# Kernel optimization log

Hardware: AMD Instinct MI355X
Metric: run time of the kernel (lower is better)

## Reference

```python
import jax, jax.numpy as jnp
import numpy as np

B = 65536
NQ = 8
NL = 3
FEAT = 64 * 3 * 3 + NQ  # 584


def _conv(x, w, b):
    # x: (B,C,H,W), w: (O,I,3,3), padding=1 -> SAME
    y = jax.lax.conv_general_dilated(
        x, w, window_strides=(1, 1), padding='SAME',
        dimension_numbers=('NCHW', 'OIHW', 'NCHW'))
    return y + b[None, :, None, None]


def _maxpool2(x):
    return jax.lax.reduce_window(
        x, -jnp.inf, jax.lax.max, (1, 1, 2, 2), (1, 1, 2, 2), 'VALID')


def _quantum_sim(x, qp):
    # x: (B,NQ); qp: (NL,NQ,3). Within a layer, qubit q depends only on its own
    # previous state (tanh term), so vectorize over qubits and scan over layers.
    x_next = jnp.roll(x, -1, axis=1)  # x[:, (q+1) % NQ]

    def step(q_state, rot):  # rot: (NQ,3)
        new = jnp.sin(rot[:, 0] * x) * jnp.cos(rot[:, 1] * x_next) \
              + jnp.tanh(rot[:, 2] * q_state)
        return new, None

    q0 = jnp.zeros_like(x)
    qf, _ = jax.lax.scan(step, q0, qp)
    return qf


def setup_inputs() -> dict:
    key = jax.random.key(0)
    ks = jax.random.split(key, 16)

    def w(k, shape, fan_in):
        lim = 1.0 / np.sqrt(fan_in)
        return jax.random.uniform(k, shape, jnp.float32, -lim, lim)

    return {
        'board_state': jax.random.normal(ks[0], (B, 3, 6, 6), jnp.float32),
        'target_positions': jax.random.randint(ks[1], (4, 2), 0, 6).astype(jnp.int64),
        'conv1_w': w(ks[2], (16, 3, 3, 3), 3 * 9), 'conv1_b': w(ks[3], (16,), 3 * 9),
        'conv2_w': w(ks[4], (32, 16, 3, 3), 16 * 9), 'conv2_b': w(ks[5], (32,), 16 * 9),
        'conv3_w': w(ks[6], (64, 32, 3, 3), 32 * 9), 'conv3_b': w(ks[7], (64,), 32 * 9),
        'quantum_params': jax.random.normal(ks[8], (NL, NQ, 3), jnp.float32),
        'pt_w1': w(ks[9], (FEAT, 128), FEAT), 'pt_b1': w(ks[9], (128,), FEAT),
        'pt_w2': w(ks[10], (128, 64), 128), 'pt_b2': w(ks[10], (64,), 128),
        'pt_w3': w(ks[11], (64, 2), 64), 'pt_b3': w(ks[11], (2,), 64),
        'cf_w1': w(ks[12], (FEAT, 64), FEAT), 'cf_b1': w(ks[12], (64,), FEAT),
        'cf_w2': w(ks[13], (64, 1), 64), 'cf_b2': w(ks[13], (1,), 64),
    }


def reference(board_state, target_positions,
              conv1_w, conv1_b, conv2_w, conv2_b, conv3_w, conv3_b,
              quantum_params,
              pt_w1, pt_b1, pt_w2, pt_b2, pt_w3, pt_b3,
              cf_w1, cf_b1, cf_w2, cf_b2):
    b = board_state.shape[0]
    h = jax.nn.relu(_conv(board_state, conv1_w, conv1_b))   # (B,16,6,6)
    h = jax.nn.relu(_conv(h, conv2_w, conv2_b))             # (B,32,6,6)
    h = _maxpool2(h)                                        # (B,32,3,3)
    h = jax.nn.relu(_conv(h, conv3_w, conv3_b))             # (B,64,3,3)
    conv_flat = h.reshape(b, -1)                            # (B,576)

    board_flat = board_state.reshape(b, -1)
    q_feat = _quantum_sim(board_flat[:, :NQ], quantum_params)  # (B,NQ)

    feats = jnp.concatenate([conv_flat, q_feat], axis=1)    # (B,584)

    # piece-type head (Dropout is identity in eval)
    t = jax.nn.relu(feats @ pt_w1 + pt_b1)
    t = jax.nn.relu(t @ pt_w2 + pt_b2)
    type_logits = t @ pt_w3 + pt_b3
    type_probs = jax.nn.softmax(type_logits, axis=1)        # (B,2)

    # confidence head
    c = jax.nn.relu(feats @ cf_w1 + cf_b1)
    confidence = jax.nn.sigmoid(c @ cf_w2 + cf_b2)          # (B,1)

    # target_positions never affect the math (pos_encoding unused in torch source);
    # the same probs/confidence are reported for every position.
    return jnp.concatenate([type_probs, confidence], axis=1)  # (B,3)
```

## Files before the change

kernel.cpp:

```cpp
#include <hip/hip_runtime.h>

typedef _Float16 h8 __attribute__((ext_vector_type(8)));
typedef _Float16 h4 __attribute__((ext_vector_type(4)));
typedef float f32x4 __attribute__((ext_vector_type(4)));

union HU { _Float16 h; unsigned short u; };
__device__ __forceinline__ unsigned short f2h(float f) { HU x; x.h = (_Float16)f; return x.u; }
__device__ __forceinline__ float h2f(unsigned short u) { HU x; x.u = u; return (float)x.h; }

#define MFMA16(a, b, c) __builtin_amdgcn_mfma_f32_16x16x32_f16((a), (b), (c), 0, 0, 0)

__global__ void k_prep(const float* __restrict__ w1, const float* __restrict__ w2,
                       const float* __restrict__ w3,
                       const float* __restrict__ ptw1, const float* __restrict__ cfw1,
                       const float* __restrict__ ptw2, const float* __restrict__ ptw3,
                       const float* __restrict__ cfw2,
                       unsigned short* __restrict__ w1f,
                       unsigned short* __restrict__ w2f,
                       unsigned short* __restrict__ w3f,
                       unsigned short* __restrict__ w1hd,
                       unsigned short* __restrict__ w2hd,
                       unsigned short* __restrict__ w3hd) {
    int gid = blockIdx.x * 256 + threadIdx.x;
    int gs = gridDim.x * 256;
    for (int e = gid; e < 1024; e += gs) {
        int f = e >> 9, lane = (e >> 3) & 63, j = e & 7;
        int k = ((lane >> 4) << 3) + j, oc = lane & 15;
        int r, within;
        if (f == 0) { r = k >> 4; within = k & 15; }
        else        { r = 2;      within = k; }
        int tx = within >> 2, ch = within & 3;
        float v = 0.f;
        if (tx < 3 && ch < 3) v = w1[oc * 27 + ch * 9 + r * 3 + tx];
        w1f[e] = f2h(v);
    }
    for (int e = gid; e < 9216; e += gs) {
        int j = e & 7, lane = (e >> 3) & 63, fo = e >> 9;
        int ot = fo & 1, t = fo >> 1;
        int k = ((lane >> 4) * 8) + j, oc = ot * 16 + (lane & 15);
        float v = (k < 16) ? w2[oc * 144 + k * 9 + t] : 0.f;
        w2f[e] = f2h(v);
    }
    for (int e = gid; e < 18432; e += gs) {
        int j = e & 7, lane = (e >> 3) & 63, fo = e >> 9;
        int oti = fo & 1, t = (fo >> 1) % 9, otp = (fo >> 1) / 9;
        int ic = ((lane >> 4) * 8) + j, oc = (otp * 2 + oti) * 16 + (lane & 15);
        w3f[e] = f2h(w3[oc * 288 + ic * 9 + t]);
    }
    for (int s = gid; s < 608 * 192; s += gs) {
        int k = s / 192, n = s - k * 192;
        float v = 0.f;
        if (k < 584) {
            int f = (k < 576) ? ((k & 63) * 9 + (k >> 6)) : k;
            v = (n < 128) ? ptw1[f * 128 + n] : cfw1[f * 64 + (n - 128)];
        }
        int kk = k >> 5, hi = (k & 31) >> 3, j = k & 7, nt = n >> 4;
        int e = (((kk * 12 + nt) << 6) | (hi << 4) | (n & 15)) << 3 | j;
        w1hd[e] = f2h(v);
    }
    for (int s = gid; s < 8192; s += gs) {
        int k = s >> 6, n = s & 63;
        float v = ptw2[k * 64 + n];
        int kk = k >> 5, hi = (k & 31) >> 3, j = k & 7, nt = n >> 4;
        int e = ((((kk << 2) | nt) << 6) | (hi << 4) | (n & 15)) << 3 | j;
        w2hd[e] = f2h(v);
    }
    for (int e = gid; e < 2048; e += gs) {
        int j = e & 7, lane = (e >> 3) & 63, kk = e >> 9;
        int k = kk * 32 + ((lane >> 4) * 8) + j, n = lane & 15;
        float v = 0.f;
        if (k < 64) { if (n < 2) v = ptw3[k * 2 + n]; }
        else        { if (n == 2) v = cfw2[k - 64]; }
        w3hd[e] = f2h(v);
    }
}

#define BDS4 260
#define BDH4 (16 * BDS4)
#define A1S 584
#define A2S 296
#define FTS 616
#define HSH 200
#define RA_OFF 19712
#define O_OFF 26112
#define LDSTOT 26368

__global__ __launch_bounds__(256, 3) void k_fused(
    const float* __restrict__ board,
    const float* __restrict__ b1, const float* __restrict__ b2,
    const float* __restrict__ b3, const float* __restrict__ qp,
    const unsigned short* __restrict__ w1f,
    const unsigned short* __restrict__ w2f,
    const unsigned short* __restrict__ w3f,
    const unsigned short* __restrict__ w1hd,
    const unsigned short* __restrict__ w2hd,
    const unsigned short* __restrict__ w3hd,
    const float* __restrict__ ptb1, const float* __restrict__ ptb2,
    const float* __restrict__ ptb3, const float* __restrict__ cfb1,
    const float* __restrict__ cfb2,
    float* __restrict__ out)
{
    __shared__ __align__(16) unsigned short LDSH[LDSTOT];
    const int tid = threadIdx.x, wid = tid >> 6, lane = tid & 63;
    const int g = wid >> 1, w2 = wid & 1;
    const int col = lane & 15, q = lane >> 4;
    const long long gg0 = (long long)blockIdx.x * 32;
    const f32x4 ZERO4 = {0.f, 0.f, 0.f, 0.f};

    unsigned short* A1 = LDSH + g * 9856;
    unsigned short* A2 = A1;
    unsigned short* Hb = LDSH + RA_OFF;
    float* O = (float*)(LDSH + O_OFF);

    for (int e = tid; e < BDH4 / 4; e += 256)
        ((unsigned long long*)(LDSH + RA_OFF))[e] = 0ULL;
    __syncthreads();

    float qv[2];
    h8 w1r0 = ((const h8*)w1f)[lane];
    h8 w1r1 = ((const h8*)w1f)[64 + lane];
    float b1v = b1[col];
    #pragma unroll
    for (int gi = 0; gi < 2; gi++) {
        for (int e = tid; e < 16 * 108; e += 256) {
            int ss = e / 108, r2 = e % 108, ch = r2 / 36, p = r2 % 36;
            float v = board[(gg0 + gi * 16) * 108 + e];
            LDSH[RA_OFF + ss * BDS4 + ((p / 6 + 1) * 8 + (p % 6) + 1) * 4 + ch] =
                f2h(v);
        }
        __syncthreads();
        if (tid < 128) {
            int ss = tid >> 3, qq = tid & 7;
            int base = RA_OFF + ss * BDS4;
            int p8a = ((qq / 6 + 1) * 8 + (qq % 6) + 1) * 4;
            int e2 = (qq + 1) & 7;
            int p8b = ((e2 / 6 + 1) * 8 + (e2 % 6) + 1) * 4;
            float xq = h2f(LDSH[base + p8a]);
            float xn = h2f(LDSH[base + p8b]);
            float st = 0.f;
            for (int l = 0; l < 3; l++) {
                float a0 = qp[l * 24 + qq * 3], a1 = qp[l * 24 + qq * 3 + 1],
                      a2 = qp[l * 24 + qq * 3 + 2];
                st = sinf(a0 * xq) * cosf(a1 * xn) + tanhf(a2 * st);
            }
            qv[gi] = st;
        }
        {
            unsigned short* A1g = LDSH + gi * 9856;
            const int bs = RA_OFF + col * BDS4;
            const int rsel = q >> 1, wo = (q & 1) * 8;
            for (int p = wid * 9; p < wid * 9 + 9; p++) {
                int y = p / 6, x = p % 6;
                int ab1 = bs + ((y + rsel) * 8 + x) * 4 + wo;
                int ab2 = bs + ((y + 2) * 8 + x) * 4 + wo;
                union { h8 v; h4 h[2]; } a1v, a2v;
                a1v.h[0] = *(const h4*)&LDSH[ab1];
                a1v.h[1] = *(const h4*)&LDSH[ab1 + 4];
                a2v.h[0] = *(const h4*)&LDSH[ab2];
                a2v.h[1] = *(const h4*)&LDSH[ab2 + 4];
                f32x4 c = MFMA16(a1v.v, w1r0, ZERO4);
                c = MFMA16(a2v.v, w1r1, c);
                #pragma unroll
                for (int r = 0; r < 4; r++)
                    A1g[(q * 4 + r) * A1S + p * 16 + col] =
                        f2h(fmaxf(c[r] + b1v, 0.f));
            }
        }
        __syncthreads();
    }

    f32x4 pooled2[9];
    #pragma unroll
    for (int pp = 0; pp < 9; pp++) pooled2[pp] = ZERO4;
    {
        h8 W2r[9];
        #pragma unroll
        for (int t = 0; t < 9; t++)
            W2r[t] = ((const h8*)w2f)[(t * 2 + w2) * 64 + lane];
        float b2v = b2[w2 * 16 + col];
        const int sA1 = col * A1S;
        const int kho = (q & 1) * 8;

        h8 R[3][6];
        #pragma unroll
        for (int x = 0; x < 6; x++) {
            R[0][x] = *(const h8*)&A1[sA1 + (0 * 6 + x) * 16 + kho];
            R[1][x] = *(const h8*)&A1[sA1 + (1 * 6 + x) * 16 + kho];
        }
        #pragma unroll
        for (int y = 0; y < 6; y++) {
            if (y >= 1 && y <= 4) {
                const int nr = y + 1, slot = nr % 3;
                #pragma unroll
                for (int x = 0; x < 6; x++)
                    R[slot][x] = *(const h8*)&A1[sA1 + (nr * 6 + x) * 16 + kho];
            }
            f32x4 acc[6];
            #pragma unroll
            for (int x = 0; x < 6; x++) acc[x] = ZERO4;
            #pragma unroll
            for (int dy = -1; dy <= 1; dy++) {
                const int ry = y + dy;
                if (ry < 0 || ry > 5) continue;
                const int slot = ry % 3;
                #pragma unroll
                for (int x = 0; x < 6; x++)
                    #pragma unroll
                    for (int dx = -1; dx <= 1; dx++) {
                        const int sx = x + dx;
                        if (sx < 0 || sx > 5) continue;
                        acc[x] = MFMA16(R[slot][sx],
                                        W2r[(dy + 1) * 3 + (dx + 1)], acc[x]);
                    }
            }
            const int pr = y >> 1;
            #pragma unroll
            for (int px = 0; px < 3; px++)
                #pragma unroll
                for (int xx = 0; xx < 2; xx++)
                    #pragma unroll
                    for (int r = 0; r < 4; r++)
                        pooled2[pr * 3 + px][r] =
                            fmaxf(pooled2[pr * 3 + px][r],
                                  acc[px * 2 + xx][r] + b2v);
        }
    }
    __syncthreads();
    #pragma unroll
    for (int pp = 0; pp < 9; pp++)
        #pragma unroll
        for (int r = 0; r < 4; r++)
            A2[(q * 4 + r) * A2S + pp * 32 + w2 * 16 + col] =
                f2h(pooled2[pp][r]);
    __syncthreads();

    f32x4 c3a[9], c3b[9];
    {
        const int otp = w2;
        const int sA2 = col * A2S;
        h8 W3r[18];
        #pragma unroll
        for (int f = 0; f < 18; f++)
            W3r[f] = ((const h8*)w3f)[(otp * 18 + f) * 64 + lane];
        #pragma unroll
        for (int p = 0; p < 9; p++) {
            const int y = p / 3, x = p % 3;
            f32x4 acc0 = ZERO4, acc1 = ZERO4;
            #pragma unroll
            for (int t = 0; t < 9; t++) {
                const int sy = y + t / 3 - 1, sx = x + t % 3 - 1;
                if (sy < 0 || sy >= 3 || sx < 0 || sx >= 3) continue;
                h8 a = *(const h8*)&A2[sA2 + (sy * 3 + sx) * 32 + q * 8];
                acc0 = MFMA16(a, W3r[t * 2 + 0], acc0);
                acc1 = MFMA16(a, W3r[t * 2 + 1], acc1);
            }
            c3a[p] = acc0; c3b[p] = acc1;
        }
    }
    __syncthreads();

    {
        const int otp = w2;
        float b3v0 = b3[(otp * 2 + 0) * 16 + col];
        float b3v1 = b3[(otp * 2 + 1) * 16 + col];
        int oc0 = (otp * 2 + 0) * 16 + col, oc1 = (otp * 2 + 1) * 16 + col;
        #pragma unroll
        for (int p = 0; p < 9; p++)
            #pragma unroll
            for (int r = 0; r < 4; r++) {
                int row = g * 16 + q * 4 + r;
                LDSH[row * FTS + p * 64 + oc0] = f2h(fmaxf(c3a[p][r] + b3v0, 0.f));
                LDSH[row * FTS + p * 64 + oc1] = f2h(fmaxf(c3b[p][r] + b3v1, 0.f));
            }
        if (tid < 128) {
            int ss = tid >> 3, qq = tid & 7;
            LDSH[ss * FTS + 576 + qq] = f2h(qv[0]);
            LDSH[(ss + 16) * FTS + 576 + qq] = f2h(qv[1]);
        }
        for (int e = tid; e < 1024; e += 256)
            LDSH[(e >> 5) * FTS + 584 + (e & 31)] = 0;
    }
    __syncthreads();

    {
        f32x4 acc[2][3];
        #pragma unroll
        for (int mt = 0; mt < 2; mt++)
            #pragma unroll
            for (int nt = 0; nt < 3; nt++) acc[mt][nt] = ZERO4;
        const h8* wp1 = (const h8*)w1hd;
        const int ntb = wid * 3;
        for (int kk = 0; kk < 19; kk++) {
            h8 a0 = *(const h8*)&LDSH[col * FTS + kk * 32 + q * 8];
            h8 a1 = *(const h8*)&LDSH[(16 + col) * FTS + kk * 32 + q * 8];
            h8 b[3];
            #pragma unroll
            for (int nt = 0; nt < 3; nt++)
                b[nt] = wp1[(kk * 12 + ntb + nt) * 64 + lane];
            #pragma unroll
            for (int nt = 0; nt < 3; nt++) {
                acc[0][nt] = MFMA16(a0, b[nt], acc[0][nt]);
                acc[1][nt] = MFMA16(a1, b[nt], acc[1][nt]);
            }
        }
        #pragma unroll
        for (int nt = 0; nt < 3; nt++) {
            int ntg = ntb + nt;
            float bv = (ntg < 8) ? ptb1[ntg * 16 + col] : cfb1[(ntg - 8) * 16 + col];
            #pragma unroll
            for (int mt = 0; mt < 2; mt++)
                #pragma unroll
                for (int r = 0; r < 4; r++)
                    Hb[(mt * 16 + q * 4 + r) * HSH + ntg * 16 + col] =
                        f2h(fmaxf(acc[mt][nt][r] + bv, 0.f));
        }
    }
    __syncthreads();

    {
        f32x4 acc2[2];
        acc2[0] = ZERO4; acc2[1] = ZERO4;
        const h8* wp2 = (const h8*)w2hd;
        const int nt2 = wid;
        #pragma unroll
        for (int kk = 0; kk < 4; kk++) {
            h8 a0 = *(const h8*)&Hb[col * HSH + kk * 32 + q * 8];
            h8 a1 = *(const h8*)&Hb[(16 + col) * HSH + kk * 32 + q * 8];
            h8 b = wp2[(kk * 4 + nt2) * 64 + lane];
            acc2[0] = MFMA16(a0, b, acc2[0]);
            acc2[1] = MFMA16(a1, b, acc2[1]);
        }
        __syncthreads();
        float bv2 = ptb2[nt2 * 16 + col];
        #pragma unroll
        for (int mt = 0; mt < 2; mt++)
            #pragma unroll
            for (int r = 0; r < 4; r++)
                Hb[(mt * 16 + q * 4 + r) * HSH + nt2 * 16 + col] =
                    f2h(fmaxf(acc2[mt][r] + bv2, 0.f));
    }
    __syncthreads();

    if (wid < 2) {
        const int mt = wid;
        f32x4 a3 = ZERO4;
        #pragma unroll
        for (int kk = 0; kk < 4; kk++) {
            int base = (kk < 2) ? kk * 32 : kk * 32 + 64;
            h8 a = *(const h8*)&Hb[(mt * 16 + col) * HSH + base + q * 8];
            h8 b = ((const h8*)w3hd)[kk * 64 + lane];
            a3 = MFMA16(a, b, a3);
        }
        if (col < 3) {
            float bv = (col < 2) ? ptb3[col] : cfb2[0];
            #pragma unroll
            for (int r = 0; r < 4; r++)
                O[(mt * 16 + q * 4 + r) * 4 + col] = a3[r] + bv;
        }
        if (lane < 16) {
            int s = mt * 16 + lane;
            float l0 = O[s * 4 + 0], l1 = O[s * 4 + 1], l2 = O[s * 4 + 2];
            float m = fmaxf(l0, l1);
            float e0 = expf(l0 - m), e1 = expf(l1 - m);
            float inv = 1.f / (e0 + e1);
            float* op = out + (gg0 + s) * 3;
            op[0] = e0 * inv;
            op[1] = e1 * inv;
            op[2] = 1.f / (1.f + expf(-l2));
        }
    }
}

extern "C" void kernel_launch(void* const* d_in, const int* in_sizes, int n_in,
                              void* d_out, int out_size, void* d_ws, size_t ws_size,
                              hipStream_t stream) {
    const float* board = (const float*)d_in[0];
    const float* c1w  = (const float*)d_in[2];
    const float* c1b  = (const float*)d_in[3];
    const float* c2w  = (const float*)d_in[4];
    const float* c2b  = (const float*)d_in[5];
    const float* c3w  = (const float*)d_in[6];
    const float* c3b  = (const float*)d_in[7];
    const float* qp   = (const float*)d_in[8];
    const float* ptw1 = (const float*)d_in[9];
    const float* ptb1 = (const float*)d_in[10];
    const float* ptw2 = (const float*)d_in[11];
    const float* ptb2 = (const float*)d_in[12];
    const float* ptw3 = (const float*)d_in[13];
    const float* ptb3 = (const float*)d_in[14];
    const float* cfw1 = (const float*)d_in[15];
    const float* cfb1 = (const float*)d_in[16];
    const float* cfw2 = (const float*)d_in[17];
    const float* cfb2 = (const float*)d_in[18];
    float* out = (float*)d_out;

    int Btot = in_sizes[0] / 108;

    unsigned short* w1f   = (unsigned short*)d_ws;
    unsigned short* w2f   = (unsigned short*)((char*)d_ws + 2048);
    unsigned short* w3f   = (unsigned short*)((char*)d_ws + 20480);
    unsigned short* w1hd  = (unsigned short*)((char*)d_ws + 57344);
    unsigned short* w2hd  = (unsigned short*)((char*)d_ws + 290816);
    unsigned short* w3hd  = (unsigned short*)((char*)d_ws + 307200);

    hipLaunchKernelGGL(k_prep, dim3(256), dim3(256), 0, stream,
                       c1w, c2w, c3w, ptw1, cfw1, ptw2, ptw3, cfw2,
                       w1f, w2f, w3f, w1hd, w2hd, w3hd);
    hipLaunchKernelGGL(k_fused, dim3(Btot / 32), dim3(256), 0, stream,
                       board, c1b, c2b, c3b, qp, w1f, w2f, w3f,
                       w1hd, w2hd, w3hd, ptb1, ptb2, ptb3, cfb1, cfb2, out);
}
```

Baseline: 175.6 us.

## Use 512-thread blocks and 32x32 MFMA for conv2 with fused pooling

Doubles the block to 8 waves and reassigns work across all stages. Conv2 now uses 32x32x16 MFMA with the 32 samples as the M dimension and K=16 input channels, so the zero-padded half of the K dimension is no longer computed. Each wave computes one pooled output position, and wave 0 also takes the ninth. Conv3 and the head GEMMs are split so each wave handles a single output or row tile. The aim is more parallelism per block and less wasted MFMA work. In exchange, conv2 no longer reuses rows through registers and the work is unevenly balanced across waves, with wave 0 doing double duty.

```diff
diff --git a/kernel.cpp b/kernel.cpp
--- a/kernel.cpp
+++ b/kernel.cpp
@@ -3,12 +3,14 @@
 typedef _Float16 h8 __attribute__((ext_vector_type(8)));
 typedef _Float16 h4 __attribute__((ext_vector_type(4)));
 typedef float f32x4 __attribute__((ext_vector_type(4)));
+typedef float f32x16 __attribute__((ext_vector_type(16)));
 
 union HU { _Float16 h; unsigned short u; };
 __device__ __forceinline__ unsigned short f2h(float f) { HU x; x.h = (_Float16)f; return x.u; }
 __device__ __forceinline__ float h2f(unsigned short u) { HU x; x.u = u; return (float)x.h; }
 
 #define MFMA16(a, b, c) __builtin_amdgcn_mfma_f32_16x16x32_f16((a), (b), (c), 0, 0, 0)
+#define MFMA32(a, b, c) __builtin_amdgcn_mfma_f32_32x32x16_f16((a), (b), (c), 0, 0, 0)
 
 __global__ void k_prep(const float* __restrict__ w1, const float* __restrict__ w2,
                        const float* __restrict__ w3,
@@ -34,12 +36,10 @@
         if (tx < 3 && ch < 3) v = w1[oc * 27 + ch * 9 + r * 3 + tx];
         w1f[e] = f2h(v);
     }
-    for (int e = gid; e < 9216; e += gs) {
-        int j = e & 7, lane = (e >> 3) & 63, fo = e >> 9;
-        int ot = fo & 1, t = fo >> 1;
-        int k = ((lane >> 4) * 8) + j, oc = ot * 16 + (lane & 15);
-        float v = (k < 16) ? w2[oc * 144 + k * 9 + t] : 0.f;
-        w2f[e] = f2h(v);
+    for (int e = gid; e < 4608; e += gs) {
+        int j = e & 7, lane = (e >> 3) & 63, t = e >> 9;
+        int oc = lane & 31, k = ((lane >> 5) << 3) + j;
+        w2f[e] = f2h(w2[oc * 144 + k * 9 + t]);
     }
     for (int e = gid; e < 18432; e += gs) {
         int j = e & 7, lane = (e >> 3) & 63, fo = e >> 9;
@@ -85,7 +85,40 @@
 #define O_OFF 26112
 #define LDSTOT 26368
 
-__global__ __launch_bounds__(256, 3) void k_fused(
+__device__ __forceinline__ f32x16 conv2_pool(const unsigned short* __restrict__ Ab,
+                                             const h8 (&W2r)[9], int kh, float b2v,
+                                             int pr, int pc) {
+    f32x16 pool;
+    #pragma unroll
+    for (int r = 0; r < 16; r++) pool[r] = 0.f;
+    #pragma unroll
+    for (int sy = 0; sy < 2; sy++)
+        #pragma unroll
+        for (int sx = 0; sx < 2; sx++) {
+            const int oy = pr * 2 + sy, ox = pc * 2 + sx;
+            f32x16 acc;
+            #pragma unroll
+            for (int r = 0; r < 16; r++) acc[r] = 0.f;
+            #pragma unroll
+            for (int dy = -1; dy <= 1; dy++) {
+                const int ry = oy + dy;
+                if (ry < 0 || ry > 5) continue;
+                #pragma unroll
+                for (int dx = -1; dx <= 1; dx++) {
+                    const int rx = ox + dx;
+                    if (rx < 0 || rx > 5) continue;
+                    h8 a = *(const h8*)&Ab[(ry * 6 + rx) * 16 + kh * 8];
+                    acc = MFMA32(a, W2r[(dy + 1) * 3 + (dx + 1)], acc);
+                }
+            }
+            #pragma unroll
+            for (int r = 0; r < 16; r++)
+                pool[r] = fmaxf(pool[r], acc[r] + b2v);
+        }
+    return pool;
+}
+
+__global__ __launch_bounds__(512, 6) void k_fused(
     const float* __restrict__ board,
     const float* __restrict__ b1, const float* __restrict__ b2,
     const float* __restrict__ b3, const float* __restrict__ qp,
@@ -102,17 +135,14 @@
 {
     __shared__ __align__(16) unsigned short LDSH[LDSTOT];
     const int tid = threadIdx.x, wid = tid >> 6, lane = tid & 63;
-    const int g = wid >> 1, w2 = wid & 1;
     const int col = lane & 15, q = lane >> 4;
     const long long gg0 = (long long)blockIdx.x * 32;
     const f32x4 ZERO4 = {0.f, 0.f, 0.f, 0.f};
 
-    unsigned short* A1 = LDSH + g * 9856;
-    unsigned short* A2 = A1;
     unsigned short* Hb = LDSH + RA_OFF;
     float* O = (float*)(LDSH + O_OFF);
 
-    for (int e = tid; e < BDH4 / 4; e += 256)
+    for (int e = tid; e < BDH4 / 4; e += 512)
         ((unsigned long long*)(LDSH + RA_OFF))[e] = 0ULL;
     __syncthreads();
 
@@ -122,8 +152,9 @@
     float b1v = b1[col];
     #pragma unroll
     for (int gi = 0; gi < 2; gi++) {
-        for (int e = tid; e < 16 * 108; e += 256) {
-            int ss = e / 108, r2 = e % 108, ch = r2 / 36, p = r2 % 36;
+        for (int e = tid; e < 16 * 108; e += 512) {
+            int r2 = e % 108, ch = r2 / 36, p = r2 % 36;
+            int ss = e / 108;
             float v = board[(gg0 + gi * 16) * 108 + e];
             LDSH[RA_OFF + ss * BDS4 + ((p / 6 + 1) * 8 + (p % 6) + 1) * 4 + ch] =
                 f2h(v);
@@ -149,7 +180,9 @@
             unsigned short* A1g = LDSH + gi * 9856;
             const int bs = RA_OFF + col * BDS4;
             const int rsel = q >> 1, wo = (q & 1) * 8;
-            for (int p = wid * 9; p < wid * 9 + 9; p++) {
+            const int p0 = wid * 4 + (wid < 4 ? wid : 4);
+            const int pe = p0 + (wid < 4 ? 5 : 4);
+            for (int p = p0; p < pe; p++) {
                 int y = p / 6, x = p % 6;
                 int ab1 = bs + ((y + rsel) * 8 + x) * 4 + wo;
                 int ab2 = bs + ((y + 2) * 8 + x) * 4 + wo;
@@ -169,138 +202,95 @@
         __syncthreads();
     }
 
-    f32x4 pooled2[9];
-    #pragma unroll
-    for (int pp = 0; pp < 9; pp++) pooled2[pp] = ZERO4;
     {
         h8 W2r[9];
         #pragma unroll
         for (int t = 0; t < 9; t++)
-            W2r[t] = ((const h8*)w2f)[(t * 2 + w2) * 64 + lane];
-        float b2v = b2[w2 * 16 + col];
-        const int sA1 = col * A1S;
-        const int kho = (q & 1) * 8;
-
-        h8 R[3][6];
-        #pragma unroll
-        for (int x = 0; x < 6; x++) {
-            R[0][x] = *(const h8*)&A1[sA1 + (0 * 6 + x) * 16 + kho];
-            R[1][x] = *(const h8*)&A1[sA1 + (1 * 6 + x) * 16 + kho];
-        }
-        #pragma unroll
-        for (int y = 0; y < 6; y++) {
-            if (y >= 1 && y <= 4) {
-                const int nr = y + 1, slot = nr % 3;
-                #pragma unroll
-                for (int x = 0; x < 6; x++)
-                    R[slot][x] = *(const h8*)&A1[sA1 + (nr * 6 + x) * 16 + kho];
-            }
-            f32x4 acc[6];
-            #pragma unroll
-            for (int x = 0; x < 6; x++) acc[x] = ZERO4;
-            #pragma unroll
-            for (int dy = -1; dy <= 1; dy++) {
-                const int ry = y + dy;
-                if (ry < 0 || ry > 5) continue;
-                const int slot = ry % 3;
-                #pragma unroll
-                for (int x = 0; x < 6; x++)
-                    #pragma unroll
-                    for (int dx = -1; dx <= 1; dx++) {
-                        const int sx = x + dx;
-                        if (sx < 0 || sx > 5) continue;
-                        acc[x] = MFMA16(R[slot][sx],
-                                        W2r[(dy + 1) * 3 + (dx + 1)], acc[x]);
-                    }
-            }
-            const int pr = y >> 1;
-            #pragma unroll
-            for (int px = 0; px < 3; px++)
-                #pragma unroll
-                for (int xx = 0; xx < 2; xx++)
-                    #pragma unroll
-                    for (int r = 0; r < 4; r++)
-                        pooled2[pr * 3 + px][r] =
-                            fmaxf(pooled2[pr * 3 + px][r],
-                                  acc[px * 2 + xx][r] + b2v);
-        }
-    }
-    __syncthreads();
-    #pragma unroll
-    for (int pp = 0; pp < 9; pp++)
-        #pragma unroll
-        for (int r = 0; r < 4; r++)
-            A2[(q * 4 + r) * A2S + pp * 32 + w2 * 16 + col] =
-                f2h(pooled2[pp][r]);
-    __syncthreads();
-
-    f32x4 c3a[9], c3b[9];
-    {
-        const int otp = w2;
+            W2r[t] = ((const h8*)w2f)[t * 64 + lane];
+        const int m32 = lane & 31, kh = lane >> 5;
+        const float b2v = b2[m32];
+        const unsigned short* Ab = LDSH + (m32 >> 4) * 9856 + (m32 & 15) * A1S;
+
+        if (wid == 0) {
+            f32x16 p8 = conv2_pool(Ab, W2r, kh, b2v, 2, 2);
+            #pragma unroll
+            for (int r = 0; r < 16; r++) {
+                int s = (r & 3) + 8 * (r >> 2) + 4 * kh;
+                LDSH[RA_OFF + s * 32 + m32] = f2h(p8[r]);
+            }
+        }
+        f32x16 pool = conv2_pool(Ab, W2r, kh, b2v, wid / 3, wid % 3);
+        __syncthreads();
+        #pragma unroll
+        for (int r = 0; r < 16; r++) {
+            int s = (r & 3) + 8 * (r >> 2) + 4 * kh;
+            LDSH[(s >> 4) * 9856 + (s & 15) * A2S + wid * 32 + m32] = f2h(pool[r]);
+        }
+        for (int e = tid; e < 1024; e += 512) {
+            int s = e >> 5;
+            LDSH[(s >> 4) * 9856 + (s & 15) * A2S + 8 * 32 + (e & 31)] =
+                LDSH[RA_OFF + e];
+        }
+    }
+    __syncthreads();
+
+    f32x4 c3[9];
+    {
+        const int g3 = wid >> 2, ot = wid & 3;
+        const unsigned short* A2g = LDSH + g3 * 9856;
+        h8 W3r[9];
+        #pragma unroll
+        for (int t = 0; t < 9; t++)
+            W3r[t] = ((const h8*)w3f)[((ot >> 1) * 18 + t * 2 + (ot & 1)) * 64 + lane];
         const int sA2 = col * A2S;
-        h8 W3r[18];
-        #pragma unroll
-        for (int f = 0; f < 18; f++)
-            W3r[f] = ((const h8*)w3f)[(otp * 18 + f) * 64 + lane];
         #pragma unroll
         for (int p = 0; p < 9; p++) {
             const int y = p / 3, x = p % 3;
-            f32x4 acc0 = ZERO4, acc1 = ZERO4;
+            f32x4 acc = ZERO4;
             #pragma unroll
             for (int t = 0; t < 9; t++) {
                 const int sy = y + t / 3 - 1, sx = x + t % 3 - 1;
                 if (sy < 0 || sy >= 3 || sx < 0 || sx >= 3) continue;
-                h8 a = *(const h8*)&A2[sA2 + (sy * 3 + sx) * 32 + q * 8];
-                acc0 = MFMA16(a, W3r[t * 2 + 0], acc0);
-                acc1 = MFMA16(a, W3r[t * 2 + 1], acc1);
-            }
-            c3a[p] = acc0; c3b[p] = acc1;
-        }
-    }
-    __syncthreads();
-
-    {
-        const int otp = w2;
-        float b3v0 = b3[(otp * 2 + 0) * 16 + col];
-        float b3v1 = b3[(otp * 2 + 1) * 16 + col];
-        int oc0 = (otp * 2 + 0) * 16 + col, oc1 = (otp * 2 + 1) * 16 + col;
+                h8 a = *(const h8*)&A2g[sA2 + (sy * 3 + sx) * 32 + q * 8];
+                acc = MFMA16(a, W3r[t], acc);
+            }
+            c3[p] = acc;
+        }
+    }
+    __syncthreads();
+
+    {
+        const int g3 = wid >> 2, ot = wid & 3;
+        float b3v = b3[ot * 16 + col];
         #pragma unroll
         for (int p = 0; p < 9; p++)
             #pragma unroll
             for (int r = 0; r < 4; r++) {
-                int row = g * 16 + q * 4 + r;
-                LDSH[row * FTS + p * 64 + oc0] = f2h(fmaxf(c3a[p][r] + b3v0, 0.f));
-                LDSH[row * FTS + p * 64 + oc1] = f2h(fmaxf(c3b[p][r] + b3v1, 0.f));
+                int row = g3 * 16 + q * 4 + r;
+                LDSH[row * FTS + p * 64 + ot * 16 + col] =
+                    f2h(fmaxf(c3[p][r] + b3v, 0.f));
             }
         if (tid < 128) {
             int ss = tid >> 3, qq = tid & 7;
             LDSH[ss * FTS + 576 + qq] = f2h(qv[0]);
             LDSH[(ss + 16) * FTS + 576 + qq] = f2h(qv[1]);
         }
-        for (int e = tid; e < 1024; e += 256)
+        for (int e = tid; e < 1024; e += 512)
             LDSH[(e >> 5) * FTS + 584 + (e & 31)] = 0;
     }
     __syncthreads();
 
     {
-        f32x4 acc[2][3];
-        #pragma unroll
-        for (int mt = 0; mt < 2; mt++)
-            #pragma unroll
-            for (int nt = 0; nt < 3; nt++) acc[mt][nt] = ZERO4;
+        f32x4 acc[3];
+        acc[0] = ZERO4; acc[1] = ZERO4; acc[2] = ZERO4;
         const h8* wp1 = (const h8*)w1hd;
-        const int ntb = wid * 3;
+        const int mt = wid & 1, ntb = (wid >> 1) * 3;
         for (int kk = 0; kk < 19; kk++) {
-            h8 a0 = *(const h8*)&LDSH[col * FTS + kk * 32 + q * 8];
-            h8 a1 = *(const h8*)&LDSH[(16 + col) * FTS + kk * 32 + q * 8];
-            h8 b[3];
-            #pragma unroll
-            for (int nt = 0; nt < 3; nt++)
-                b[nt] = wp1[(kk * 12 + ntb + nt) * 64 + lane];
+            h8 a = *(const h8*)&LDSH[(mt * 16 + col) * FTS + kk * 32 + q * 8];
             #pragma unroll
             for (int nt = 0; nt < 3; nt++) {
-                acc[0][nt] = MFMA16(a0, b[nt], acc[0][nt]);
-                acc[1][nt] = MFMA16(a1, b[nt], acc[1][nt]);
+                h8 b = wp1[(kk * 12 + ntb + nt) * 64 + lane];
+                acc[nt] = MFMA16(a, b, acc[nt]);
             }
         }
         #pragma unroll
@@ -308,36 +298,29 @@
             int ntg = ntb + nt;
             float bv = (ntg < 8) ? ptb1[ntg * 16 + col] : cfb1[(ntg - 8) * 16 + col];
             #pragma unroll
-            for (int mt = 0; mt < 2; mt++)
-                #pragma unroll
-                for (int r = 0; r < 4; r++)
-                    Hb[(mt * 16 + q * 4 + r) * HSH + ntg * 16 + col] =
-                        f2h(fmaxf(acc[mt][nt][r] + bv, 0.f));
-        }
-    }
-    __syncthreads();
-
-    {
-        f32x4 acc2[2];
-        acc2[0] = ZERO4; acc2[1] = ZERO4;
+            for (int r = 0; r < 4; r++)
+                Hb[(mt * 16 + q * 4 + r) * HSH + ntg * 16 + col] =
+                    f2h(fmaxf(acc[nt][r] + bv, 0.f));
+        }
+    }
+    __syncthreads();
+
+    {
+        f32x4 acc2 = ZERO4;
         const h8* wp2 = (const h8*)w2hd;
-        const int nt2 = wid;
+        const int mt = wid & 1, nt2 = wid >> 1;
         #pragma unroll
         for (int kk = 0; kk < 4; kk++) {
-            h8 a0 = *(const h8*)&Hb[col * HSH + kk * 32 + q * 8];
-            h8 a1 = *(const h8*)&Hb[(16 + col) * HSH + kk * 32 + q * 8];
+            h8 a = *(const h8*)&Hb[(mt * 16 + col) * HSH + kk * 32 + q * 8];
             h8 b = wp2[(kk * 4 + nt2) * 64 + lane];
-            acc2[0] = MFMA16(a0, b, acc2[0]);
-            acc2[1] = MFMA16(a1, b, acc2[1]);
+            acc2 = MFMA16(a, b, acc2);
         }
         __syncthreads();
         float bv2 = ptb2[nt2 * 16 + col];
         #pragma unroll
-        for (int mt = 0; mt < 2; mt++)
-            #pragma unroll
-            for (int r = 0; r < 4; r++)
-                Hb[(mt * 16 + q * 4 + r) * HSH + nt2 * 16 + col] =
-                    f2h(fmaxf(acc2[mt][r] + bv2, 0.f));
+        for (int r = 0; r < 4; r++)
+            Hb[(mt * 16 + q * 4 + r) * HSH + nt2 * 16 + col] =
+                f2h(fmaxf(acc2[r] + bv2, 0.f));
     }
     __syncthreads();
 
@@ -406,7 +389,7 @@
     hipLaunchKernelGGL(k_prep, dim3(256), dim3(256), 0, stream,
                        c1w, c2w, c3w, ptw1, cfw1, ptw2, ptw3, cfw2,
                        w1f, w2f, w3f, w1hd, w2hd, w3hd);
-    hipLaunchKernelGGL(k_fused, dim3(Btot / 32), dim3(256), 0, stream,
+    hipLaunchKernelGGL(k_fused, dim3(Btot / 32), dim3(512), 0, stream,
                        board, c1b, c2b, c3b, qp, w1f, w2f, w3f,
                        w1hd, w2hd, w3hd, ptb1, ptb2, ptb3, cfb1, cfb2, out);
 }
```

After: 295.8 us. 1.69x slower.

## Rewrite conv2 with 32x32 MFMA per pooled cell and vectorize board loads

Applied to the files above, without the earlier changes.

Conv2 is restructured to use 32x32x16 MFMA tiles: each wave computes whole pooled output cells (all 32 output channels for 32 samples) instead of a row-sliding 16x16 scheme, and the weight prep layout is changed to match. The board load uses float4 reads, the head's layer-2 output goes to a separate LDS region so one barrier can be dropped, and s_setprio hints wrap the MFMA-heavy loops. The cost is uneven wave work (one wave computes three pool cells) and more A1 LDS reads, since row registers are no longer reused.

```diff
diff --git a/kernel.cpp b/kernel.cpp
--- a/kernel.cpp
+++ b/kernel.cpp
@@ -3,12 +3,14 @@
 typedef _Float16 h8 __attribute__((ext_vector_type(8)));
 typedef _Float16 h4 __attribute__((ext_vector_type(4)));
 typedef float f32x4 __attribute__((ext_vector_type(4)));
+typedef float f32x16 __attribute__((ext_vector_type(16)));
 
 union HU { _Float16 h; unsigned short u; };
 __device__ __forceinline__ unsigned short f2h(float f) { HU x; x.h = (_Float16)f; return x.u; }
 __device__ __forceinline__ float h2f(unsigned short u) { HU x; x.u = u; return (float)x.h; }
 
 #define MFMA16(a, b, c) __builtin_amdgcn_mfma_f32_16x16x32_f16((a), (b), (c), 0, 0, 0)
+#define MFMA32(a, b, c) __builtin_amdgcn_mfma_f32_32x32x16_f16((a), (b), (c), 0, 0, 0)
 
 __global__ void k_prep(const float* __restrict__ w1, const float* __restrict__ w2,
                        const float* __restrict__ w3,
@@ -34,12 +36,10 @@
         if (tx < 3 && ch < 3) v = w1[oc * 27 + ch * 9 + r * 3 + tx];
         w1f[e] = f2h(v);
     }
-    for (int e = gid; e < 9216; e += gs) {
-        int j = e & 7, lane = (e >> 3) & 63, fo = e >> 9;
-        int ot = fo & 1, t = fo >> 1;
-        int k = ((lane >> 4) * 8) + j, oc = ot * 16 + (lane & 15);
-        float v = (k < 16) ? w2[oc * 144 + k * 9 + t] : 0.f;
-        w2f[e] = f2h(v);
+    for (int e = gid; e < 4608; e += gs) {
+        int j = e & 7, lane = (e >> 3) & 63, t = e >> 9;
+        int oc = lane & 31, k = ((lane >> 5) << 3) + j;
+        w2f[e] = f2h(w2[oc * 144 + k * 9 + t]);
     }
     for (int e = gid; e < 18432; e += gs) {
         int j = e & 7, lane = (e >> 3) & 63, fo = e >> 9;
@@ -84,6 +84,39 @@
 #define RA_OFF 19712
 #define O_OFF 26112
 #define LDSTOT 26368
+
+__device__ __forceinline__ f32x16 conv2_pool(const unsigned short* __restrict__ Ab,
+                                             const h8 (&W2r)[9], int kh, float b2v,
+                                             int pr, int pc) {
+    f32x16 pool;
+    #pragma unroll
+    for (int r = 0; r < 16; r++) pool[r] = 0.f;
+    #pragma unroll
+    for (int sy = 0; sy < 2; sy++)
+        #pragma unroll
+        for (int sx = 0; sx < 2; sx++) {
+            const int oy = pr * 2 + sy, ox = pc * 2 + sx;
+            f32x16 acc;
+            #pragma unroll
+            for (int r = 0; r < 16; r++) acc[r] = 0.f;
+            #pragma unroll
+            for (int dy = -1; dy <= 1; dy++) {
+                const int ry = oy + dy;
+                if (ry < 0 || ry > 5) continue;
+                #pragma unroll
+                for (int dx = -1; dx <= 1; dx++) {
+                    const int rx = ox + dx;
+                    if (rx < 0 || rx > 5) continue;
+                    h8 a = *(const h8*)&Ab[(ry * 6 + rx) * 16 + kh * 8];
+                    acc = MFMA32(a, W2r[(dy + 1) * 3 + (dx + 1)], acc);
+                }
+            }
+            #pragma unroll
+            for (int r = 0; r < 16; r++)
+                pool[r] = fmaxf(pool[r], acc[r] + b2v);
+        }
+    return pool;
+}
 
 __global__ __launch_bounds__(256, 3) void k_fused(
     const float* __restrict__ board,
@@ -122,11 +155,17 @@
     float b1v = b1[col];
     #pragma unroll
     for (int gi = 0; gi < 2; gi++) {
-        for (int e = tid; e < 16 * 108; e += 256) {
-            int ss = e / 108, r2 = e % 108, ch = r2 / 36, p = r2 % 36;
-            float v = board[(gg0 + gi * 16) * 108 + e];
-            LDSH[RA_OFF + ss * BDS4 + ((p / 6 + 1) * 8 + (p % 6) + 1) * 4 + ch] =
-                f2h(v);
+        for (int e4 = tid; e4 < 432; e4 += 256) {
+            int ss = e4 / 27, r27 = e4 - ss * 27;
+            const float* bp = board + (gg0 + gi * 16 + ss) * 108;
+            f32x4 v = ((const f32x4*)bp)[r27];
+            int f0 = r27 * 4;
+            #pragma unroll
+            for (int j = 0; j < 4; j++) {
+                int f = f0 + j, ch = f / 36, p = f - ch * 36;
+                LDSH[RA_OFF + ss * BDS4 + ((p / 6 + 1) * 8 + (p % 6) + 1) * 4 + ch] =
+                    f2h(v[j]);
+            }
         }
         __syncthreads();
         if (tid < 128) {
@@ -169,69 +208,38 @@
         __syncthreads();
     }
 
-    f32x4 pooled2[9];
-    #pragma unroll
-    for (int pp = 0; pp < 9; pp++) pooled2[pp] = ZERO4;
     {
         h8 W2r[9];
         #pragma unroll
         for (int t = 0; t < 9; t++)
-            W2r[t] = ((const h8*)w2f)[(t * 2 + w2) * 64 + lane];
-        float b2v = b2[w2 * 16 + col];
-        const int sA1 = col * A1S;
-        const int kho = (q & 1) * 8;
-
-        h8 R[3][6];
-        #pragma unroll
-        for (int x = 0; x < 6; x++) {
-            R[0][x] = *(const h8*)&A1[sA1 + (0 * 6 + x) * 16 + kho];
-            R[1][x] = *(const h8*)&A1[sA1 + (1 * 6 + x) * 16 + kho];
-        }
-        #pragma unroll
-        for (int y = 0; y < 6; y++) {
-            if (y >= 1 && y <= 4) {
-                const int nr = y + 1, slot = nr % 3;
-                #pragma unroll
-                for (int x = 0; x < 6; x++)
-                    R[slot][x] = *(const h8*)&A1[sA1 + (nr * 6 + x) * 16 + kho];
-            }
-            f32x4 acc[6];
-            #pragma unroll
-            for (int x = 0; x < 6; x++) acc[x] = ZERO4;
-            #pragma unroll
-            for (int dy = -1; dy <= 1; dy++) {
-                const int ry = y + dy;
-                if (ry < 0 || ry > 5) continue;
-                const int slot = ry % 3;
-                #pragma unroll
-                for (int x = 0; x < 6; x++)
-                    #pragma unroll
-                    for (int dx = -1; dx <= 1; dx++) {
-                        const int sx = x + dx;
-                        if (sx < 0 || sx > 5) continue;
-                        acc[x] = MFMA16(R[slot][sx],
-                                        W2r[(dy + 1) * 3 + (dx + 1)], acc[x]);
-                    }
-            }
-            const int pr = y >> 1;
-            #pragma unroll
-            for (int px = 0; px < 3; px++)
-                #pragma unroll
-                for (int xx = 0; xx < 2; xx++)
-                    #pragma unroll
-                    for (int r = 0; r < 4; r++)
-                        pooled2[pr * 3 + px][r] =
-                            fmaxf(pooled2[pr * 3 + px][r],
-                                  acc[px * 2 + xx][r] + b2v);
-        }
-    }
-    __syncthreads();
-    #pragma unroll
-    for (int pp = 0; pp < 9; pp++)
-        #pragma unroll
-        for (int r = 0; r < 4; r++)
-            A2[(q * 4 + r) * A2S + pp * 32 + w2 * 16 + col] =
-                f2h(pooled2[pp][r]);
+            W2r[t] = ((const h8*)w2f)[t * 64 + lane];
+        const int m32 = lane & 31, kh = lane >> 5;
+        const float b2v = b2[m32];
+        const unsigned short* Ab = LDSH + (m32 >> 4) * 9856 + (m32 & 15) * A1S;
+
+        __builtin_amdgcn_s_setprio(1);
+        f32x16 pA = conv2_pool(Ab, W2r, kh, b2v, wid / 3, wid % 3);
+        const int cB = wid + 4;
+        f32x16 pB = conv2_pool(Ab, W2r, kh, b2v, cB / 3, cB % 3);
+        f32x16 pC;
+        if (wid == 3) pC = conv2_pool(Ab, W2r, kh, b2v, 2, 2);
+        __builtin_amdgcn_s_setprio(0);
+        __syncthreads();
+        #pragma unroll
+        for (int r = 0; r < 16; r++) {
+            int s = (r & 3) + 8 * (r >> 2) + 4 * kh;
+            int rb = (s >> 4) * 9856 + (s & 15) * A2S + m32;
+            LDSH[rb + wid * 32] = f2h(pA[r]);
+            LDSH[rb + cB * 32]  = f2h(pB[r]);
+        }
+        if (wid == 3) {
+            #pragma unroll
+            for (int r = 0; r < 16; r++) {
+                int s = (r & 3) + 8 * (r >> 2) + 4 * kh;
+                LDSH[(s >> 4) * 9856 + (s & 15) * A2S + 8 * 32 + m32] = f2h(pC[r]);
+            }
+        }
+    }
     __syncthreads();
 
     f32x4 c3a[9], c3b[9];
@@ -242,6 +250,7 @@
         #pragma unroll
         for (int f = 0; f < 18; f++)
             W3r[f] = ((const h8*)w3f)[(otp * 18 + f) * 64 + lane];
+        __builtin_amdgcn_s_setprio(1);
         #pragma unroll
         for (int p = 0; p < 9; p++) {
             const int y = p / 3, x = p % 3;
@@ -256,6 +265,7 @@
             }
             c3a[p] = acc0; c3b[p] = acc1;
         }
+        __builtin_amdgcn_s_setprio(0);
     }
     __syncthreads();
 
@@ -290,6 +300,7 @@
             for (int nt = 0; nt < 3; nt++) acc[mt][nt] = ZERO4;
         const h8* wp1 = (const h8*)w1hd;
         const int ntb = wid * 3;
+        __builtin_amdgcn_s_setprio(1);
         for (int kk = 0; kk < 19; kk++) {
             h8 a0 = *(const h8*)&LDSH[col * FTS + kk * 32 + q * 8];
             h8 a1 = *(const h8*)&LDSH[(16 + col) * FTS + kk * 32 + q * 8];
@@ -303,6 +314,7 @@
                 acc[1][nt] = MFMA16(a1, b[nt], acc[1][nt]);
             }
         }
+        __builtin_amdgcn_s_setprio(0);
         #pragma unroll
         for (int nt = 0; nt < 3; nt++) {
             int ntg = ntb + nt;
@@ -330,13 +342,12 @@
             acc2[0] = MFMA16(a0, b, acc2[0]);
             acc2[1] = MFMA16(a1, b, acc2[1]);
         }
-        __syncthreads();
         float bv2 = ptb2[nt2 * 16 + col];
         #pragma unroll
         for (int mt = 0; mt < 2; mt++)
             #pragma unroll
             for (int r = 0; r < 4; r++)
-                Hb[(mt * 16 + q * 4 + r) * HSH + nt2 * 16 + col] =
+                LDSH[(mt * 16 + q * 4 + r) * HSH + nt2 * 16 + col] =
                     f2h(fmaxf(acc2[mt][r] + bv2, 0.f));
     }
     __syncthreads();
@@ -346,8 +357,9 @@
         f32x4 a3 = ZERO4;
         #pragma unroll
         for (int kk = 0; kk < 4; kk++) {
-            int base = (kk < 2) ? kk * 32 : kk * 32 + 64;
-            h8 a = *(const h8*)&Hb[(mt * 16 + col) * HSH + base + q * 8];
+            h8 a = (kk < 2)
+                ? *(const h8*)&LDSH[(mt * 16 + col) * HSH + kk * 32 + q * 8]
+                : *(const h8*)&Hb[(mt * 16 + col) * HSH + kk * 32 + 64 + q * 8];
             h8 b = ((const h8*)w3hd)[kk * 64 + lane];
             a3 = MFMA16(a, b, a3);
         }
```

Result: slower. 264.9 us (+50.9%).
